# Optimization experiments

Measured on AMD Instinct MI355X. Metric: run time of the kernel, lower is better.

Reference implementation:

```python
import jax, jax.numpy as jnp
import numpy as np

N = 100000      # n_nodes
E = 1600000     # n_edges (avg degree 16)
D_IN, D_H, D_OUT = 128, 64, 16


def setup_inputs() -> dict:
    key = jax.random.key(0)
    k1, k2, k3, k4 = jax.random.split(key, 4)
    x = jax.random.normal(k1, (N, D_IN), dtype=jnp.float32)
    edge_index = jax.random.randint(k2, (2, E), 0, N, dtype=jnp.int32)
    W1 = jax.random.normal(k3, (D_IN, D_H), dtype=jnp.float32) / np.sqrt(D_IN)
    b1 = jnp.zeros((D_H,), dtype=jnp.float32)
    W2 = jax.random.normal(k4, (D_H, D_OUT), dtype=jnp.float32) / np.sqrt(D_H)
    b2 = jnp.zeros((D_OUT,), dtype=jnp.float32)
    return {"x": x, "edge_index": edge_index, "W1": W1, "b1": b1, "W2": W2, "b2": b2}


def gcn_conv(x, src, dst, W, b, n):
    """PyG GCNConv: linear transform, then deg^-1/2 A deg^-1/2 aggregation, + bias.
    src/dst already include self-loops."""
    h = x @ W                                              # [n, d_out]
    deg = jax.ops.segment_sum(jnp.ones_like(dst, dtype=h.dtype), dst, num_segments=n)
    dinv = jnp.where(deg > 0, jax.lax.rsqrt(jnp.maximum(deg, 1.0)), 0.0)
    norm = dinv[src] * dinv[dst]                           # [E+n]
    msgs = h[src] * norm[:, None]                          # gather + scale
    out = jax.ops.segment_sum(msgs, dst, num_segments=n)   # scatter-add
    return out + b


def reference(x, edge_index, W1, b1, W2, b2):
    loops = jnp.arange(N, dtype=edge_index.dtype)
    src = jnp.concatenate([edge_index[0], loops])
    dst = jnp.concatenate([edge_index[1], loops])
    h = jax.nn.relu(gcn_conv(x, src, dst, W1, b1, N))
    return gcn_conv(h, src, dst, W2, b2, N)
```

## Files before the change

kernel.cpp:

```cpp
#include <hip/hip_runtime.h>
#include <cstdint>

#define N_NODES 100000
#define N_EDGES 1600000
#define D_IN    128
#define D_H     64
#define D_OUT   16
#define M_TILES 6250

#define NBKT   512
#define NPB    196
#define BCAP   4096
#define TILE_E 4096
#define NTILES ((N_EDGES + TILE_E - 1) / TILE_E)
#define G1     256
#define GEMM_BLOCKS ((M_TILES + 3) / 4)

typedef __attribute__((ext_vector_type(8))) short short8;
typedef __attribute__((ext_vector_type(4))) float floatx4;

static __device__ __forceinline__ unsigned short f2bf(float f) {
    unsigned int u = __float_as_uint(f);
    u = u + 0x7FFFu + ((u >> 16) & 1u);
    return (unsigned short)(u >> 16);
}
static __device__ __forceinline__ float bf2f(unsigned short h) {
    return __uint_as_float(((unsigned int)h) << 16);
}


__global__ __launch_bounds__(512) void zero_small_kernel(int* __restrict__ cursors,
                                                         int* __restrict__ srcs) {
    cursors[threadIdx.x] = 0;
    if (threadIdx.x < 16) srcs[N_EDGES + threadIdx.x] = 0;
}

__global__ __launch_bounds__(256) void fused_bin_gemm1_kernel(
        const int* __restrict__ src, const int* __restrict__ dst,
        int* __restrict__ cursors, int* __restrict__ region,
        const float* __restrict__ x, const float* __restrict__ W1,
        float* __restrict__ h_raw) {
    __shared__ int hcnt[NBKT];
    __shared__ int hbase[NBKT];
    __shared__ unsigned short bhi_lds[8192];
    __shared__ unsigned short blo_lds[8192];

    const int t = threadIdx.x;

    if (blockIdx.x < G1) {
        for (int tile = blockIdx.x; tile < NTILES; tile += G1) {
            for (int i = t; i < NBKT; i += 256) hcnt[i] = 0;
            __syncthreads();
            int e0 = tile * TILE_E + t * 16;
            int pk[16], bk[16], rk[16];
            bool full = (e0 + 16 <= N_EDGES);
            if (full) {
                const int4* dp = (const int4*)(dst + e0);
                const int4* sp = (const int4*)(src + e0);
                int dv[16], sv[16];
                #pragma unroll
                for (int q = 0; q < 4; ++q) {
                    int4 d4 = dp[q]; int4 s4 = sp[q];
                    dv[4*q+0]=d4.x; dv[4*q+1]=d4.y; dv[4*q+2]=d4.z; dv[4*q+3]=d4.w;
                    sv[4*q+0]=s4.x; sv[4*q+1]=s4.y; sv[4*q+2]=s4.z; sv[4*q+3]=s4.w;
                }
                #pragma unroll
                for (int k = 0; k < 16; ++k) {
                    int d = dv[k];
                    int b = d / NPB;
                    bk[k] = b;
                    pk[k] = ((d - b * NPB) << 17) | sv[k];
                    rk[k] = atomicAdd(&hcnt[b], 1);
                }
            }
            __syncthreads();
            for (int i = t; i < NBKT; i += 256) {
                int c = hcnt[i];
                if (c > 0) hbase[i] = atomicAdd(&cursors[i], c);
            }
            __syncthreads();
            if (full) {
                #pragma unroll
                for (int k = 0; k < 16; ++k)
                    region[bk[k] * BCAP + hbase[bk[k]] + rk[k]] = pk[k];
            }
            __syncthreads();
        }
        return;
    }

    for (int e = t; e < 8192; e += 256) {
        int j    = e & 7;
        int lane = (e >> 3) & 63;
        int pair = e >> 9;
        int kc   = pair >> 2;
        int nt   = pair & 3;
        int k = kc * 32 + (lane >> 4) * 8 + j;
        int n = nt * 16 + (lane & 15);
        float w = W1[k * D_H + n];
        unsigned short hi = f2bf(w);
        float lo = w - bf2f(hi);
        bhi_lds[e] = hi;
        blo_lds[e] = f2bf(lo);
    }
    __syncthreads();

    int wid  = t >> 6;
    int lane = t & 63;
    int quad = lane >> 4;
    int m    = lane & 15;

    int tile = (blockIdx.x - G1) * 4 + wid;
    if (tile >= M_TILES) return;
    int mbase = tile * 16;

    const float* xr = x + (size_t)(mbase + m) * D_IN + quad * 8;
    short8 ahi[4], alo[4];
    #pragma unroll
    for (int kc = 0; kc < 4; ++kc) {
        floatx4 v0 = *(const floatx4*)(xr + kc * 32);
        floatx4 v1 = *(const floatx4*)(xr + kc * 32 + 4);
        float f[8] = {v0.x, v0.y, v0.z, v0.w, v1.x, v1.y, v1.z, v1.w};
        #pragma unroll
        for (int j = 0; j < 8; ++j) {
            unsigned short hi = f2bf(f[j]);
            float lo = f[j] - bf2f(hi);
            ahi[kc][j] = (short)hi;
            alo[kc][j] = (short)f2bf(lo);
        }
    }

    floatx4 acc[4] = {{0.f,0.f,0.f,0.f},{0.f,0.f,0.f,0.f},{0.f,0.f,0.f,0.f},{0.f,0.f,0.f,0.f}};
    #pragma unroll
    for (int kc = 0; kc < 4; ++kc) {
        #pragma unroll
        for (int nt = 0; nt < 4; ++nt) {
            int fo = ((kc * 4 + nt) * 64 + lane) * 8;
            short8 bhi = *(const short8*)&bhi_lds[fo];
            short8 blo = *(const short8*)&blo_lds[fo];
            acc[nt] = __builtin_amdgcn_mfma_f32_16x16x32_bf16(ahi[kc], bhi, acc[nt], 0, 0, 0);
            acc[nt] = __builtin_amdgcn_mfma_f32_16x16x32_bf16(ahi[kc], blo, acc[nt], 0, 0, 0);
            acc[nt] = __builtin_amdgcn_mfma_f32_16x16x32_bf16(alo[kc], bhi, acc[nt], 0, 0, 0);
        }
    }

    #pragma unroll
    for (int nt = 0; nt < 4; ++nt) {
        int col = nt * 16 + m;
        #pragma unroll
        for (int r = 0; r < 4; ++r) {
            int row = mbase + quad * 4 + r;
            h_raw[(size_t)row * D_H + col] = acc[nt][r];
        }
    }
}

__global__ __launch_bounds__(256) void build_kernel(const int* __restrict__ cursors,
                                                    const int* __restrict__ region,
                                                    int* __restrict__ offsets,
                                                    float* __restrict__ dinv,
                                                    int* __restrict__ srcs,
                                                    const float* __restrict__ h_raw,
                                                    unsigned short* __restrict__ hs) {
    __shared__ int lhist[NPB];
    __shared__ int lscan[NPB + 1];
    __shared__ int sbuf[256];
    __shared__ int srt[BCAP];
    __shared__ int red[4];
    __shared__ float sdv[NPB];
    int b = blockIdx.x;
    int t = threadIdx.x;

    int c0 = cursors[t];
    int c1 = cursors[t + 256];
    int p = ((t < b) ? c0 : 0) + ((t + 256 < b) ? c1 : 0);
    int lane = t & 63, wid = t >> 6;
    #pragma unroll
    for (int off = 32; off > 0; off >>= 1) p += __shfl_down(p, off);
    if (lane == 0) red[wid] = p;
    __syncthreads();
    int base = red[0] + red[1] + red[2] + red[3];
    int cnt = cursors[b];
    const int* reg = region + b * BCAP;

    for (int i = t; i < NPB; i += 256) lhist[i] = 0;
    __syncthreads();
    for (int i = t; i < cnt; i += 256) {
        int ln = reg[i] >> 17;
        atomicAdd(&lhist[ln], 1);
    }
    __syncthreads();
    int v = (t < NPB) ? lhist[t] : 0;
    sbuf[t] = v;
    __syncthreads();
    for (int off = 1; off < 256; off <<= 1) {
        int u = (t >= off) ? sbuf[t - off] : 0;
        __syncthreads();
        sbuf[t] += u;
        __syncthreads();
    }
    int incl = sbuf[t];
    if (t < NPB) lscan[t] = incl - v;
    if (t == NPB - 1) lscan[NPB] = incl;
    __syncthreads();
    if (t < NPB) lhist[t] = incl - v;
    __syncthreads();

    int node0 = b * NPB;
    int nlim = N_NODES - node0;
    if (nlim > NPB) nlim = NPB;
    if (t < nlim) {
        offsets[node0 + t] = base + lscan[t];
        int c = lscan[t + 1] - lscan[t];
        float dvv = rsqrtf((float)c + 1.0f);
        dinv[node0 + t] = dvv;
        sdv[t] = dvv;
    }
    if (b == (N_NODES - 1) / NPB && t == 0) offsets[N_NODES] = base + cnt;

    for (int i = t; i < cnt; i += 256) {
        int pk = reg[i];
        int ln = pk >> 17;
        int pos = atomicAdd(&lhist[ln], 1);
        srt[pos] = pk & 0x1FFFF;
    }
    __syncthreads();
    for (int i = t; i < cnt; i += 256) srcs[base + i] = srt[i];

    int tot = nlim * D_H;
    for (int i = t; i < tot; i += 256) {
        int r = i >> 6;
        int c = i & 63;
        size_t off = (size_t)(node0 + r) * D_H + c;
        hs[off] = f2bf(h_raw[off] * sdv[r]);
    }
}

__global__ __launch_bounds__(256) void agg1_fused_kernel(const unsigned short* __restrict__ hs,
                                                         const int* __restrict__ offsets,
                                                         const int* __restrict__ srcs,
                                                         const float* __restrict__ dinv,
                                                         const float* __restrict__ b1,
                                                         const float* __restrict__ W2,
                                                         float* __restrict__ h2s) {
    __shared__ float w2t[16 * 68];
    __shared__ float rbuf[16 * 68];

    const int tid = threadIdx.x;
    for (int i = tid; i < 1024; i += 256) {
        int j = i >> 4, c = i & 15;
        w2t[c * 68 + j] = W2[i];
    }

    const int g    = tid >> 4;
    const int sl   = tid & 15;
    const int node = blockIdx.x * 16 + g;
    const int c4   = sl * 4;

    const int beg = offsets[node];
    const int end = offsets[node + 1];

    ushort4 s4v = *(const ushort4*)(hs + (size_t)node * D_H + c4);
    float a0 = bf2f(s4v.x), a1 = bf2f(s4v.y), a2 = bf2f(s4v.z), a3 = bf2f(s4v.w);

    for (int e = beg; e < end; e += 16) {
        int rem = end - e;
        int idx = srcs[e + sl];
        #pragma unroll
        for (int k = 0; k < 16; ++k) {
            int j = __shfl(idx, k, 16);
            ushort4 v = *(const ushort4*)(hs + (size_t)j * D_H + c4);
            float m = (k < rem) ? 1.0f : 0.0f;
            a0 = fmaf(bf2f(v.x), m, a0);
            a1 = fmaf(bf2f(v.y), m, a1);
            a2 = fmaf(bf2f(v.z), m, a2);
            a3 = fmaf(bf2f(v.w), m, a3);
        }
    }

    const float dv = dinv[node];
    const floatx4 bb = *(const floatx4*)(b1 + c4);
    float* rb = rbuf + g * 68;
    rb[c4 + 0] = fmaxf(a0 * dv + bb.x, 0.f);
    rb[c4 + 1] = fmaxf(a1 * dv + bb.y, 0.f);
    rb[c4 + 2] = fmaxf(a2 * dv + bb.z, 0.f);
    rb[c4 + 3] = fmaxf(a3 * dv + bb.w, 0.f);
    __syncthreads();

    float p = 0.f;
    #pragma unroll
    for (int t4 = 0; t4 < 16; ++t4) {
        floatx4 rv = *(const floatx4*)(rb + 4 * t4);
        floatx4 wv = *(const floatx4*)(&w2t[sl * 68 + 4 * t4]);
        p += rv.x * wv.x + rv.y * wv.y + rv.z * wv.z + rv.w * wv.w;
    }
    h2s[node * D_OUT + sl] = p * dv;
}

__global__ __launch_bounds__(256) void agg2_kernel(const float* __restrict__ h2s,
                                                   const int* __restrict__ offsets,
                                                   const int* __restrict__ srcs,
                                                   const float* __restrict__ dinv,
                                                   const float* __restrict__ b2,
                                                   float* __restrict__ out) {
    int col = threadIdx.x & 15;
    int nidx = (blockIdx.x * blockDim.x + threadIdx.x) >> 4;
    int stride = (gridDim.x * blockDim.x) >> 4;
    for (int node = nidx; node < N_NODES; node += stride) {
        int beg = offsets[node], end = offsets[node + 1];
        float acc = h2s[node * D_OUT + col];
        for (int e = beg; e < end; e += 16) {
            int rem = end - e;
            const int* ep = srcs + e;
            int jj[16];
            #pragma unroll
            for (int k = 0; k < 16; ++k) jj[k] = ep[k];
            float vv[16];
            #pragma unroll
            for (int k = 0; k < 16; ++k) vv[k] = h2s[jj[k] * D_OUT + col];
            #pragma unroll
            for (int k = 0; k < 16; ++k) {
                float m = (k < rem) ? 1.0f : 0.0f;
                acc = fmaf(vv[k], m, acc);
            }
        }
        out[node * D_OUT + col] = acc * dinv[node] + b2[col];
    }
}

extern "C" void kernel_launch(void* const* d_in, const int* in_sizes, int n_in,
                              void* d_out, int out_size, void* d_ws, size_t ws_size,
                              hipStream_t stream) {
    const float* x  = (const float*)d_in[0];
    const int*   ei = (const int*)d_in[1];
    const float* W1 = (const float*)d_in[2];
    const float* b1 = (const float*)d_in[3];
    const float* W2 = (const float*)d_in[4];
    const float* b2 = (const float*)d_in[5];
    float* out = (float*)d_out;

    const int* src = ei;
    const int* dst = ei + N_EDGES;

    char* w = (char*)d_ws;
    int*   cursors  = (int*)(w + 0);
    int*   offsets  = (int*)(w + 4096);
    float* dinv     = (float*)(w + 404224);
    int*   srcs     = (int*)(w + 804224);
    unsigned short* hs = (unsigned short*)(w + 7204352);
    float* h2s      = (float*)(w + 20004480);
    int*   region   = (int*)(w + 26404480);
    float* h_raw    = (float*)(w + 34793088);

    zero_small_kernel<<<1, 512, 0, stream>>>(cursors, srcs);
    fused_bin_gemm1_kernel<<<G1 + GEMM_BLOCKS, 256, 0, stream>>>(
        src, dst, cursors, region, x, W1, h_raw);
    build_kernel<<<NBKT, 256, 0, stream>>>(cursors, region, offsets, dinv, srcs,
                                           h_raw, hs);
    agg1_fused_kernel<<<6250, 256, 0, stream>>>(hs, offsets, srcs, dinv, b1, W2, h2s);
    agg2_kernel<<<6250, 256, 0, stream>>>(h2s, offsets, srcs, dinv, b2, out);
}
```

Baseline: 199.3 us.

## Column-slice feature layouts so gathers stay L2-resident, one thread per node

Stores the scaled bf16 hidden features as 8 column slices of 8 values per node, and the second-layer features as 4 slices of 4 floats. The aggregation kernels now assign one thread per node per slice, so each gather pass touches a small slice that can fit in cache and avoids the masked 16-wide loop. Layer-1 aggregation is split from the W2 projection, which now runs as a separate kernel reading an fp32 intermediate. This costs an extra kernel launch, an extra write and read of a 100000x64 fp32 buffer, and per-thread serial edge loops with divergent degrees.

Result: slower. 362.2 us (+81.8%).

```diff
diff --git a/kernel.cpp b/kernel.cpp
--- a/kernel.cpp
+++ b/kernel.cpp
@@ -15,6 +15,10 @@
 #define NTILES ((N_EDGES + TILE_E - 1) / TILE_E)
 #define G1     256
 #define GEMM_BLOCKS ((M_TILES + 3) / 4)
+#define NCHUNK 391
+
+#define HS_SLICE   (N_NODES * 8)
+#define H2S_SLICE  (N_NODES * 4)
 
 typedef __attribute__((ext_vector_type(8))) short short8;
 typedef __attribute__((ext_vector_type(4))) float floatx4;
@@ -161,7 +165,7 @@
                                                     float* __restrict__ dinv,
                                                     int* __restrict__ srcs,
                                                     const float* __restrict__ h_raw,
-                                                    unsigned short* __restrict__ hs) {
+                                                    unsigned short* __restrict__ hs_cs) {
     __shared__ int lhist[NPB];
     __shared__ int lscan[NPB + 1];
     __shared__ int sbuf[256];
@@ -227,22 +231,60 @@
     __syncthreads();
     for (int i = t; i < cnt; i += 256) srcs[base + i] = srt[i];
 
-    int tot = nlim * D_H;
+    int tot = nlim * 16;
     for (int i = t; i < tot; i += 256) {
-        int r = i >> 6;
-        int c = i & 63;
-        size_t off = (size_t)(node0 + r) * D_H + c;
-        hs[off] = f2bf(h_raw[off] * sdv[r]);
-    }
-}
-
-__global__ __launch_bounds__(256) void agg1_fused_kernel(const unsigned short* __restrict__ hs,
-                                                         const int* __restrict__ offsets,
-                                                         const int* __restrict__ srcs,
-                                                         const float* __restrict__ dinv,
-                                                         const float* __restrict__ b1,
-                                                         const float* __restrict__ W2,
-                                                         float* __restrict__ h2s) {
+        int r  = i >> 4;
+        int q  = i & 15;
+        int cg = q >> 1;
+        int sub = (q & 1) * 4;
+        int row = node0 + r;
+        floatx4 hv = *(const floatx4*)(h_raw + (size_t)row * D_H + cg * 8 + sub);
+        float s = sdv[r];
+        ushort4 o;
+        o.x = f2bf(hv.x * s); o.y = f2bf(hv.y * s);
+        o.z = f2bf(hv.z * s); o.w = f2bf(hv.w * s);
+        *(ushort4*)(hs_cs + (size_t)cg * HS_SLICE + (size_t)row * 8 + sub) = o;
+    }
+}
+
+__global__ __launch_bounds__(256) void agg1a_kernel(const unsigned short* __restrict__ hs_cs,
+                                                    const int* __restrict__ offsets,
+                                                    const int* __restrict__ srcs,
+                                                    float* __restrict__ agg_raw) {
+    const int cg    = blockIdx.x & 7;
+    const int chunk = blockIdx.x >> 3;
+    const int node  = chunk * 256 + threadIdx.x;
+    if (node >= N_NODES) return;
+
+    const unsigned short* slice = hs_cs + (size_t)cg * HS_SLICE;
+    const int beg = offsets[node];
+    const int end = offsets[node + 1];
+
+    ushort4 s0 = *(const ushort4*)(slice + (size_t)node * 8);
+    ushort4 s1 = *(const ushort4*)(slice + (size_t)node * 8 + 4);
+    float a0 = bf2f(s0.x), a1 = bf2f(s0.y), a2 = bf2f(s0.z), a3 = bf2f(s0.w);
+    float a4 = bf2f(s1.x), a5 = bf2f(s1.y), a6 = bf2f(s1.z), a7 = bf2f(s1.w);
+
+    for (int e = beg; e < end; ++e) {
+        int j = srcs[e];
+        ushort4 v0 = *(const ushort4*)(slice + (size_t)j * 8);
+        ushort4 v1 = *(const ushort4*)(slice + (size_t)j * 8 + 4);
+        a0 += bf2f(v0.x); a1 += bf2f(v0.y); a2 += bf2f(v0.z); a3 += bf2f(v0.w);
+        a4 += bf2f(v1.x); a5 += bf2f(v1.y); a6 += bf2f(v1.z); a7 += bf2f(v1.w);
+    }
+
+    float* o = agg_raw + (size_t)node * D_H + cg * 8;
+    floatx4 w0 = {a0, a1, a2, a3};
+    floatx4 w1 = {a4, a5, a6, a7};
+    *(floatx4*)(o)     = w0;
+    *(floatx4*)(o + 4) = w1;
+}
+
+__global__ __launch_bounds__(256) void proj_kernel(const float* __restrict__ agg_raw,
+                                                   const float* __restrict__ dinv,
+                                                   const float* __restrict__ b1,
+                                                   const float* __restrict__ W2,
+                                                   float* __restrict__ h2s_cs) {
     __shared__ float w2t[16 * 68];
     __shared__ float rbuf[16 * 68];
 
@@ -257,34 +299,14 @@
     const int node = blockIdx.x * 16 + g;
     const int c4   = sl * 4;
 
-    const int beg = offsets[node];
-    const int end = offsets[node + 1];
-
-    ushort4 s4v = *(const ushort4*)(hs + (size_t)node * D_H + c4);
-    float a0 = bf2f(s4v.x), a1 = bf2f(s4v.y), a2 = bf2f(s4v.z), a3 = bf2f(s4v.w);
-
-    for (int e = beg; e < end; e += 16) {
-        int rem = end - e;
-        int idx = srcs[e + sl];
-        #pragma unroll
-        for (int k = 0; k < 16; ++k) {
-            int j = __shfl(idx, k, 16);
-            ushort4 v = *(const ushort4*)(hs + (size_t)j * D_H + c4);
-            float m = (k < rem) ? 1.0f : 0.0f;
-            a0 = fmaf(bf2f(v.x), m, a0);
-            a1 = fmaf(bf2f(v.y), m, a1);
-            a2 = fmaf(bf2f(v.z), m, a2);
-            a3 = fmaf(bf2f(v.w), m, a3);
-        }
-    }
-
     const float dv = dinv[node];
+    floatx4 av = *(const floatx4*)(agg_raw + (size_t)node * D_H + c4);
     const floatx4 bb = *(const floatx4*)(b1 + c4);
     float* rb = rbuf + g * 68;
-    rb[c4 + 0] = fmaxf(a0 * dv + bb.x, 0.f);
-    rb[c4 + 1] = fmaxf(a1 * dv + bb.y, 0.f);
-    rb[c4 + 2] = fmaxf(a2 * dv + bb.z, 0.f);
-    rb[c4 + 3] = fmaxf(a3 * dv + bb.w, 0.f);
+    rb[c4 + 0] = fmaxf(av.x * dv + bb.x, 0.f);
+    rb[c4 + 1] = fmaxf(av.y * dv + bb.y, 0.f);
+    rb[c4 + 2] = fmaxf(av.z * dv + bb.z, 0.f);
+    rb[c4 + 3] = fmaxf(av.w * dv + bb.w, 0.f);
     __syncthreads();
 
     float p = 0.f;
@@ -294,38 +316,39 @@
         floatx4 wv = *(const floatx4*)(&w2t[sl * 68 + 4 * t4]);
         p += rv.x * wv.x + rv.y * wv.y + rv.z * wv.z + rv.w * wv.w;
     }
-    h2s[node * D_OUT + sl] = p * dv;
-}
-
-__global__ __launch_bounds__(256) void agg2_kernel(const float* __restrict__ h2s,
-                                                   const int* __restrict__ offsets,
-                                                   const int* __restrict__ srcs,
-                                                   const float* __restrict__ dinv,
-                                                   const float* __restrict__ b2,
-                                                   float* __restrict__ out) {
-    int col = threadIdx.x & 15;
-    int nidx = (blockIdx.x * blockDim.x + threadIdx.x) >> 4;
-    int stride = (gridDim.x * blockDim.x) >> 4;
-    for (int node = nidx; node < N_NODES; node += stride) {
-        int beg = offsets[node], end = offsets[node + 1];
-        float acc = h2s[node * D_OUT + col];
-        for (int e = beg; e < end; e += 16) {
-            int rem = end - e;
-            const int* ep = srcs + e;
-            int jj[16];
-            #pragma unroll
-            for (int k = 0; k < 16; ++k) jj[k] = ep[k];
-            float vv[16];
-            #pragma unroll
-            for (int k = 0; k < 16; ++k) vv[k] = h2s[jj[k] * D_OUT + col];
-            #pragma unroll
-            for (int k = 0; k < 16; ++k) {
-                float m = (k < rem) ? 1.0f : 0.0f;
-                acc = fmaf(vv[k], m, acc);
-            }
-        }
-        out[node * D_OUT + col] = acc * dinv[node] + b2[col];
-    }
+    h2s_cs[(size_t)(sl >> 2) * H2S_SLICE + (size_t)node * 4 + (sl & 3)] = p * dv;
+}
+
+__global__ __launch_bounds__(256) void agg2a_kernel(const float* __restrict__ h2s_cs,
+                                                    const int* __restrict__ offsets,
+                                                    const int* __restrict__ srcs,
+                                                    const float* __restrict__ dinv,
+                                                    const float* __restrict__ b2,
+                                                    float* __restrict__ out) {
+    const int cg    = blockIdx.x & 3;
+    const int chunk = blockIdx.x >> 2;
+    const int node  = chunk * 256 + threadIdx.x;
+    if (node >= N_NODES) return;
+
+    const float* slice = h2s_cs + (size_t)cg * H2S_SLICE;
+    const int beg = offsets[node];
+    const int end = offsets[node + 1];
+
+    floatx4 acc = *(const floatx4*)(slice + (size_t)node * 4);
+    for (int e = beg; e < end; ++e) {
+        int j = srcs[e];
+        floatx4 v = *(const floatx4*)(slice + (size_t)j * 4);
+        acc.x += v.x; acc.y += v.y; acc.z += v.z; acc.w += v.w;
+    }
+
+    const float dv = dinv[node];
+    const floatx4 bb = *(const floatx4*)(b2 + cg * 4);
+    floatx4 o;
+    o.x = acc.x * dv + bb.x;
+    o.y = acc.y * dv + bb.y;
+    o.z = acc.z * dv + bb.z;
+    o.w = acc.w * dv + bb.w;
+    *(floatx4*)(out + (size_t)node * D_OUT + cg * 4) = o;
 }
 
 extern "C" void kernel_launch(void* const* d_in, const int* in_sizes, int n_in,
@@ -347,16 +370,18 @@
     int*   offsets  = (int*)(w + 4096);
     float* dinv     = (float*)(w + 404224);
     int*   srcs     = (int*)(w + 804224);
-    unsigned short* hs = (unsigned short*)(w + 7204352);
-    float* h2s      = (float*)(w + 20004480);
+    unsigned short* hs_cs = (unsigned short*)(w + 7204352);
+    float* h2s_cs   = (float*)(w + 20004480);
     int*   region   = (int*)(w + 26404480);
     float* h_raw    = (float*)(w + 34793088);
+    float* agg_raw  = (float*)(w + 60393088);
 
     zero_small_kernel<<<1, 512, 0, stream>>>(cursors, srcs);
     fused_bin_gemm1_kernel<<<G1 + GEMM_BLOCKS, 256, 0, stream>>>(
         src, dst, cursors, region, x, W1, h_raw);
     build_kernel<<<NBKT, 256, 0, stream>>>(cursors, region, offsets, dinv, srcs,
-                                           h_raw, hs);
-    agg1_fused_kernel<<<6250, 256, 0, stream>>>(hs, offsets, srcs, dinv, b1, W2, h2s);
-    agg2_kernel<<<6250, 256, 0, stream>>>(h2s, offsets, srcs, dinv, b2, out);
-}
+                                           h_raw, hs_cs);
+    agg1a_kernel<<<8 * NCHUNK, 256, 0, stream>>>(hs_cs, offsets, srcs, agg_raw);
+    proj_kernel<<<6250, 256, 0, stream>>>(agg_raw, dinv, b1, W2, h2s_cs);
+    agg2a_kernel<<<4 * NCHUNK, 256, 0, stream>>>(h2s_cs, offsets, srcs, dinv, b2, out);
+}
```
